# Performance work log

Hardware: AMD Instinct MI355X
Metric: run time of the kernel (lower is better)

The kernel has to match this reference:

```python
import jax, jax.numpy as jnp
import numpy as np

N_NODES = 100_000
N_EDGES = 3_200_000
FAN_IN, FAN_MID, FAN_OUT = 512, 256, 64
NEG_SLOPE = 0.01  # F.leaky_relu default


def setup_inputs() -> dict:
    key = jax.random.key(0)
    ks = jax.random.split(key, 8)
    x = jax.random.normal(ks[0], (N_NODES, FAN_IN), dtype=jnp.float32)
    edge_src = jax.random.randint(ks[1], (N_EDGES,), 0, N_NODES, dtype=jnp.int32)
    edge_dst = jax.random.randint(ks[2], (N_EDGES,), 0, N_NODES, dtype=jnp.int32)
    edge_w1 = jax.random.uniform(ks[3], (N_EDGES,), dtype=jnp.float32)
    edge_w2 = jax.random.uniform(ks[4], (N_EDGES,), dtype=jnp.float32)
    W1 = jax.random.normal(ks[5], (FAN_IN, FAN_MID), dtype=jnp.float32) * (1.0 / np.sqrt(FAN_IN))
    b1 = jnp.zeros((FAN_MID,), dtype=jnp.float32)
    W2 = jax.random.normal(ks[6], (FAN_MID, FAN_OUT), dtype=jnp.float32) * (1.0 / np.sqrt(FAN_MID))
    b2 = jnp.zeros((FAN_OUT,), dtype=jnp.float32)
    return {"x": x, "edge_src": edge_src, "edge_dst": edge_dst,
            "edge_w1": edge_w1, "edge_w2": edge_w2,
            "W1": W1, "b1": b1, "W2": W2, "b2": b2}


def _gcn_layer(x, W, b, src, dst, ew):
    # GraphConvolution: support = x @ W ; out = A @ support + b (A sparse via edges)
    support = x @ W                                 # [N, F_out]
    msgs = support[src] * ew[:, None]               # gather + scale, [E, F_out]
    agg = jax.ops.segment_sum(msgs, dst, num_segments=x.shape[0])  # scatter-add
    return agg + b


def reference(x, edge_src, edge_dst, edge_w1, edge_w2, W1, b1, W2, b2):
    h = _gcn_layer(x, W1, b1, edge_src, edge_dst, edge_w1)
    h = jax.nn.leaky_relu(h, NEG_SLOPE)
    # dropout is identity at inference (training=False)
    h = _gcn_layer(h, W2, b2, edge_src, edge_dst, edge_w2)
    return jax.nn.log_softmax(h, axis=1)
```

## Files before the change

kernel.cpp:

```cpp
#include <hip/hip_runtime.h>
#include <stdint.h>

#define FAN_IN  512
#define FAN_MID 256
#define FAN_OUT 64
#define NEG_SLOPE 0.01f
#define NPB 128
#define MAXNB 1024
#define BPART 256

typedef __bf16 bf16_t;
typedef bf16_t bf16x8 __attribute__((ext_vector_type(8)));
typedef float  f32x4  __attribute__((ext_vector_type(4)));
typedef unsigned short u16x8 __attribute__((ext_vector_type(8)));

__device__ inline unsigned short f2b(float f) {
    union { float f; unsigned int u; } v; v.f = f;
    unsigned int u = v.u;
    return (unsigned short)((u + 0x7fffu + ((u >> 16) & 1u)) >> 16);
}
__device__ inline float b2f(unsigned short u) {
    union { unsigned int u; float f; } v; v.u = ((unsigned int)u) << 16; return v.f;
}

__global__ void zerob_kernel(int* p, int n) {
    int i = blockIdx.x * 256 + threadIdx.x;
    if (i < n) p[i] = 0;
}

__global__ __launch_bounds__(256) void part_hist(const int* __restrict__ dst,
                                                 int* __restrict__ gcount,
                                                 int* __restrict__ bcount,
                                                 int E, int nb, int chunk) {
    __shared__ int lc[MAXNB];
    int blk = blockIdx.x;
    for (int i = threadIdx.x; i < nb; i += 256) lc[i] = 0;
    __syncthreads();
    int s = blk * chunk;
    int e = s + chunk; if (e > E) e = E;
    for (int i = s + threadIdx.x; i < e; i += 256)
        atomicAdd(&lc[dst[i] >> 7], 1);
    __syncthreads();
    for (int i = threadIdx.x; i < nb; i += 256) {
        int c = lc[i];
        gcount[blk * nb + i] = c;
        if (c) atomicAdd(&bcount[i], c);
    }
}

__global__ void bscan_kernel(const int* __restrict__ bcount, int* __restrict__ boff,
                             int nb, int E) {
    __shared__ int part[1024];
    int t = threadIdx.x;
    int chunk = (nb + 1023) >> 10;
    int s = t * chunk;
    int e = s + chunk; if (e > nb) e = nb;
    int sum = 0;
    for (int i = s; i < e; i++) sum += bcount[i];
    part[t] = sum;
    __syncthreads();
    for (int off = 1; off < 1024; off <<= 1) {
        int v = (t >= off) ? part[t - off] : 0;
        __syncthreads();
        part[t] += v;
        __syncthreads();
    }
    int run = (t == 0) ? 0 : part[t - 1];
    for (int i = s; i < e; i++) {
        boff[i] = run;
        run += bcount[i];
    }
    if (t == 1023) boff[nb] = E;
}

__global__ __launch_bounds__(BPART) void part_scan(const int* __restrict__ gcount,
                                                   const int* __restrict__ boff,
                                                   int* __restrict__ gbase, int nb) {
    __shared__ int v[BPART];
    int bucket = blockIdx.x;
    int t = threadIdx.x;
    int val = gcount[t * nb + bucket];
    v[t] = val;
    __syncthreads();
    for (int off = 1; off < BPART; off <<= 1) {
        int x = (t >= off) ? v[t - off] : 0;
        __syncthreads();
        v[t] += x;
        __syncthreads();
    }
    gbase[t * nb + bucket] = (t == 0 ? 0 : v[t - 1]) + boff[bucket];
}

__global__ __launch_bounds__(256) void part_scatter(const int* __restrict__ src,
                                                    const int* __restrict__ dst,
                                                    const float* __restrict__ w1,
                                                    const float* __restrict__ w2,
                                                    const int* __restrict__ gbase,
                                                    uint4* __restrict__ bstage,
                                                    int E, int nb, int chunk) {
    __shared__ int lcur[MAXNB];
    int blk = blockIdx.x;
    for (int i = threadIdx.x; i < nb; i += 256) lcur[i] = gbase[blk * nb + i];
    __syncthreads();
    int s = blk * chunk;
    int e = s + chunk; if (e > E) e = E;
    for (int i = s + threadIdx.x; i < e; i += 256) {
        int d = dst[i];
        int pos = atomicAdd(&lcur[d >> 7], 1);
        uint4 v;
        v.x = (unsigned int)src[i];
        v.y = __float_as_uint(w1[i]);
        v.z = __float_as_uint(w2[i]);
        v.w = (unsigned int)d;
        bstage[pos] = v;
    }
}

__global__ __launch_bounds__(256) void bsort_kernel(const uint4* __restrict__ bstage,
                                                    const int* __restrict__ boff,
                                                    int* __restrict__ offsets,
                                                    uint2* __restrict__ csr1,
                                                    uint2* __restrict__ csr2,
                                                    int Nn, int E, int nb) {
    __shared__ int cnt[NPB];
    __shared__ int scn[NPB];
    __shared__ int cur[NPB];
    int b = blockIdx.x;
    int t = threadIdx.x;
    int base = boff[b], end = boff[b + 1];
    int n0 = b * NPB;
    if (t < NPB) cnt[t] = 0;
    __syncthreads();
    for (int i = base + t; i < end; i += 256)
        atomicAdd(&cnt[bstage[i].w - n0], 1);
    __syncthreads();
    if (t == 0) {
        int run = 0;
        for (int j = 0; j < NPB; j++) { scn[j] = run; run += cnt[j]; }
    }
    __syncthreads();
    if (t < NPB) {
        cur[t] = scn[t];
        int n = n0 + t;
        if (n < Nn) offsets[n] = base + scn[t];
    }
    if (b == nb - 1 && t == 0) offsets[Nn] = E;
    __syncthreads();
    for (int i = base + t; i < end; i += 256) {
        uint4 rec = bstage[i];
        int lp = atomicAdd(&cur[rec.w - n0], 1);
        uint2 r1; r1.x = rec.x; r1.y = rec.y;
        uint2 r2; r2.x = rec.x; r2.y = rec.z;
        csr1[base + lp] = r1;
        csr2[base + lp] = r2;
    }
}

__global__ void convert_w_kernel(const float* __restrict__ W, unsigned short* __restrict__ Wt,
                                 int K, int N) {
    int idx = blockIdx.x * 256 + threadIdx.x;
    if (idx >= K * N) return;
    int k = idx / N, n = idx % N;
    Wt[(size_t)n * K + k] = f2b(W[idx]);
}

template<int K, int N, bool A_F32>
__global__ __launch_bounds__(256) void gemm_bt(const void* __restrict__ Ap,
                                               const unsigned short* __restrict__ Bt,
                                               unsigned short* __restrict__ C, int M) {
    constexpr int LDT = 40;
    constexpr int NW  = N / 64;
    __shared__ unsigned short As[64 * LDT];
    __shared__ unsigned short Bs[N * LDT];
    const int m0   = blockIdx.x * 64;
    const int tid  = threadIdx.x;
    const int lane = tid & 63;
    const int w    = tid >> 6;
    const int lrow = tid >> 2;
    const int lseg = (tid & 3) * 8;
    const int q    = lane >> 4;
    const int mm   = lane & 15;

    f32x4 acc[4][NW] = {};

    for (int k0 = 0; k0 < K; k0 += 32) {
        __syncthreads();
        {
            int gm = m0 + lrow;
            u16x8 av;
            if (A_F32) {
                const float* A32 = (const float*)Ap;
                if (gm < M) {
                    const float4* pp = (const float4*)(A32 + (size_t)gm * K + k0 + lseg);
                    float4 f0 = pp[0], f1 = pp[1];
                    av[0] = f2b(f0.x); av[1] = f2b(f0.y); av[2] = f2b(f0.z); av[3] = f2b(f0.w);
                    av[4] = f2b(f1.x); av[5] = f2b(f1.y); av[6] = f2b(f1.z); av[7] = f2b(f1.w);
                } else av = (u16x8)0;
            } else {
                const unsigned short* A16 = (const unsigned short*)Ap;
                if (gm < M) av = *(const u16x8*)(A16 + (size_t)gm * K + k0 + lseg);
                else        av = (u16x8)0;
            }
            *(u16x8*)&As[lrow * LDT + lseg] = av;
        }
#pragma unroll
        for (int r = 0; r < N / 64; r++) {
            int nr = r * 64 + lrow;
            *(u16x8*)&Bs[nr * LDT + lseg] =
                *(const u16x8*)(Bt + (size_t)nr * K + k0 + lseg);
        }
        __syncthreads();

        bf16x8 a[4], b[NW];
#pragma unroll
        for (int mi = 0; mi < 4; mi++)
            a[mi] = *(const bf16x8*)&As[(mi * 16 + mm) * LDT + q * 8];
#pragma unroll
        for (int ni = 0; ni < NW; ni++)
            b[ni] = *(const bf16x8*)&Bs[(w * NW * 16 + ni * 16 + mm) * LDT + q * 8];
#pragma unroll
        for (int mi = 0; mi < 4; mi++)
#pragma unroll
            for (int ni = 0; ni < NW; ni++)
                acc[mi][ni] = __builtin_amdgcn_mfma_f32_16x16x32_bf16(a[mi], b[ni], acc[mi][ni], 0, 0, 0);
    }

#pragma unroll
    for (int mi = 0; mi < 4; mi++)
#pragma unroll
        for (int ni = 0; ni < NW; ni++)
#pragma unroll
            for (int r = 0; r < 4; r++) {
                int row = m0 + mi * 16 + q * 4 + r;
                if (row < M)
                    C[(size_t)row * N + w * NW * 16 + ni * 16 + mm] = f2b(acc[mi][ni][r]);
            }
}

__global__ __launch_bounds__(256) void agg1_kernel(const unsigned short* __restrict__ S,
                                                   const int* __restrict__ offsets,
                                                   const uint2* __restrict__ edges,
                                                   const float* __restrict__ b1,
                                                   unsigned short* __restrict__ h, int Nn) {
    int wave = threadIdx.x >> 6;
    int lane = threadIdx.x & 63;
    int node = blockIdx.x * 4 + wave;
    if (node >= Nn) return;
    int s = offsets[node], e = offsets[node + 1];
    const int half = lane >> 5;
    const int elo  = lane & 31;
    float acc[8] = {0.f, 0.f, 0.f, 0.f, 0.f, 0.f, 0.f, 0.f};
    int i = s;
    for (; i + 16 <= e; i += 16) {
        uint2 ed[8];
#pragma unroll
        for (int p = 0; p < 8; p++) ed[p] = edges[i + 2 * p + half];
        u16x8 v[8];
#pragma unroll
        for (int p = 0; p < 8; p++)
            v[p] = *(const u16x8*)(S + (size_t)ed[p].x * 256 + elo * 8);
#pragma unroll
        for (int p = 0; p < 8; p++) {
            float w = __uint_as_float(ed[p].y);
#pragma unroll
            for (int k = 0; k < 8; k++) acc[k] += w * b2f(v[p][k]);
        }
    }
    for (; i + 2 <= e; i += 2) {
        uint2 ev = edges[i + half];
        float w = __uint_as_float(ev.y);
        u16x8 v = *(const u16x8*)(S + (size_t)ev.x * 256 + elo * 8);
#pragma unroll
        for (int k = 0; k < 8; k++) acc[k] += w * b2f(v[k]);
    }
    if (i < e) {
        uint2 ev = edges[i];
        float w = half ? 0.f : __uint_as_float(ev.y);
        u16x8 v = *(const u16x8*)(S + (size_t)ev.x * 256 + elo * 8);
#pragma unroll
        for (int k = 0; k < 8; k++) acc[k] += w * b2f(v[k]);
    }
#pragma unroll
    for (int k = 0; k < 8; k++) acc[k] += __shfl_xor(acc[k], 32);
    if (half == 0) {
        float4 bb0 = ((const float4*)b1)[elo * 2];
        float4 bb1 = ((const float4*)b1)[elo * 2 + 1];
        float r[8];
        r[0] = acc[0] + bb0.x; r[1] = acc[1] + bb0.y;
        r[2] = acc[2] + bb0.z; r[3] = acc[3] + bb0.w;
        r[4] = acc[4] + bb1.x; r[5] = acc[5] + bb1.y;
        r[6] = acc[6] + bb1.z; r[7] = acc[7] + bb1.w;
        u16x8 o;
#pragma unroll
        for (int k = 0; k < 8; k++) {
            float t = r[k] > 0.f ? r[k] : r[k] * NEG_SLOPE;
            o[k] = f2b(t);
        }
        *(u16x8*)&h[(size_t)node * 256 + elo * 8] = o;
    }
}

__global__ __launch_bounds__(256) void agg2_kernel(const unsigned short* __restrict__ S,
                                                   const int* __restrict__ offsets,
                                                   const uint2* __restrict__ edges,
                                                   const float* __restrict__ b2,
                                                   float* __restrict__ out, int Nn) {
    int wave = threadIdx.x >> 6;
    int lane = threadIdx.x & 63;
    int node = blockIdx.x * 4 + wave;
    if (node >= Nn) return;
    int s = offsets[node], e = offsets[node + 1];
    const int slot = lane >> 3;
    const int fblk = lane & 7;
    float acc[8] = {0.f, 0.f, 0.f, 0.f, 0.f, 0.f, 0.f, 0.f};
    int i = s;
    for (; i + 16 <= e; i += 16) {
        uint2 e0 = edges[i + slot];
        uint2 e1 = edges[i + 8 + slot];
        u16x8 v0 = *(const u16x8*)(S + (size_t)e0.x * 64 + fblk * 8);
        u16x8 v1 = *(const u16x8*)(S + (size_t)e1.x * 64 + fblk * 8);
        float w0 = __uint_as_float(e0.y), w1 = __uint_as_float(e1.y);
#pragma unroll
        for (int k = 0; k < 8; k++) acc[k] += w0 * b2f(v0[k]) + w1 * b2f(v1[k]);
    }
    for (; i + 8 <= e; i += 8) {
        uint2 ev = edges[i + slot];
        u16x8 v = *(const u16x8*)(S + (size_t)ev.x * 64 + fblk * 8);
        float w = __uint_as_float(ev.y);
#pragma unroll
        for (int k = 0; k < 8; k++) acc[k] += w * b2f(v[k]);
    }
    int rem = e - i;
    if (rem > 0) {
        int j = i + (slot < rem ? slot : rem - 1);
        uint2 ev = edges[j];
        float w = (slot < rem) ? __uint_as_float(ev.y) : 0.f;
        u16x8 v = *(const u16x8*)(S + (size_t)ev.x * 64 + fblk * 8);
#pragma unroll
        for (int k = 0; k < 8; k++) acc[k] += w * b2f(v[k]);
    }
#pragma unroll
    for (int k = 0; k < 8; k++) {
        acc[k] += __shfl_xor(acc[k], 8);
        acc[k] += __shfl_xor(acc[k], 16);
        acc[k] += __shfl_xor(acc[k], 32);
    }
    float4 bb0 = ((const float4*)b2)[fblk * 2];
    float4 bb1 = ((const float4*)b2)[fblk * 2 + 1];
    float logit[8];
    logit[0] = acc[0] + bb0.x; logit[1] = acc[1] + bb0.y;
    logit[2] = acc[2] + bb0.z; logit[3] = acc[3] + bb0.w;
    logit[4] = acc[4] + bb1.x; logit[5] = acc[5] + bb1.y;
    logit[6] = acc[6] + bb1.z; logit[7] = acc[7] + bb1.w;
    float m = logit[0];
#pragma unroll
    for (int k = 1; k < 8; k++) m = fmaxf(m, logit[k]);
    m = fmaxf(m, __shfl_xor(m, 1));
    m = fmaxf(m, __shfl_xor(m, 2));
    m = fmaxf(m, __shfl_xor(m, 4));
    float sum = 0.f;
#pragma unroll
    for (int k = 0; k < 8; k++) sum += expf(logit[k] - m);
    sum += __shfl_xor(sum, 1);
    sum += __shfl_xor(sum, 2);
    sum += __shfl_xor(sum, 4);
    float ls = logf(sum);
    if (slot == 0) {
        float* op = out + (size_t)node * 64 + fblk * 8;
        float4 o0, o1;
        o0.x = logit[0] - m - ls; o0.y = logit[1] - m - ls;
        o0.z = logit[2] - m - ls; o0.w = logit[3] - m - ls;
        o1.x = logit[4] - m - ls; o1.y = logit[5] - m - ls;
        o1.z = logit[6] - m - ls; o1.w = logit[7] - m - ls;
        ((float4*)op)[0] = o0;
        ((float4*)op)[1] = o1;
    }
}

extern "C" void kernel_launch(void* const* d_in, const int* in_sizes, int n_in,
                              void* d_out, int out_size, void* d_ws, size_t ws_size,
                              hipStream_t stream) {
    const float* x    = (const float*)d_in[0];
    const int*   esrc = (const int*)d_in[1];
    const int*   edst = (const int*)d_in[2];
    const float* ew1  = (const float*)d_in[3];
    const float* ew2  = (const float*)d_in[4];
    const float* W1   = (const float*)d_in[5];
    const float* b1   = (const float*)d_in[6];
    const float* W2   = (const float*)d_in[7];
    const float* b2   = (const float*)d_in[8];
    float* out = (float*)d_out;
    const int Nn = in_sizes[0] / FAN_IN;
    const int E  = in_sizes[1];
    const int NB = (Nn + NPB - 1) / NPB;
    const int chunk = (E + BPART - 1) / BPART;

    char* p = (char*)d_ws;
    auto alloc = [&](size_t bytes) -> char* {
        char* r = p;
        p += (bytes + 255) & ~(size_t)255;
        return r;
    };
    size_t s1_bytes = (size_t)Nn * FAN_MID * 2;
    size_t st_bytes = (size_t)E * 16;
    char* s1_region = alloc(s1_bytes > st_bytes ? s1_bytes : st_bytes);
    unsigned short* support1 = (unsigned short*)s1_region;
    uint4*          bstage   = (uint4*)s1_region;
    unsigned short* h        = (unsigned short*)alloc((size_t)Nn * FAN_MID * 2);
    unsigned short* support2 = (unsigned short*)alloc((size_t)Nn * FAN_OUT * 2);
    unsigned short* W1t      = (unsigned short*)alloc((size_t)FAN_IN * FAN_MID * 2);
    unsigned short* W2t      = (unsigned short*)alloc((size_t)FAN_MID * FAN_OUT * 2);
    int*            bcount   = (int*)alloc((size_t)NB * 4);
    int*            boff     = (int*)alloc(((size_t)NB + 1) * 4);
    int*            gcount   = (int*)alloc((size_t)BPART * NB * 4);
    int*            gbase    = (int*)alloc((size_t)BPART * NB * 4);
    int*            offsets  = (int*)alloc(((size_t)Nn + 1) * 4);
    uint2*          csr1     = (uint2*)alloc((size_t)E * 8);
    uint2*          csr2     = (uint2*)alloc((size_t)E * 8);

    zerob_kernel<<<(NB + 255) / 256, 256, 0, stream>>>(bcount, NB);
    part_hist<<<BPART, 256, 0, stream>>>(edst, gcount, bcount, E, NB, chunk);
    bscan_kernel<<<1, 1024, 0, stream>>>(bcount, boff, NB, E);
    part_scan<<<NB, BPART, 0, stream>>>(gcount, boff, gbase, NB);
    part_scatter<<<BPART, 256, 0, stream>>>(esrc, edst, ew1, ew2, gbase, bstage, E, NB, chunk);
    bsort_kernel<<<NB, 256, 0, stream>>>(bstage, boff, offsets, csr1, csr2, Nn, E, NB);

    convert_w_kernel<<<(FAN_IN * FAN_MID + 255) / 256, 256, 0, stream>>>(W1, W1t, FAN_IN, FAN_MID);
    convert_w_kernel<<<(FAN_MID * FAN_OUT + 255) / 256, 256, 0, stream>>>(W2, W2t, FAN_MID, FAN_OUT);

    gemm_bt<FAN_IN, FAN_MID, true><<<dim3((Nn + 63) / 64, 1), 256, 0, stream>>>(
        x, W1t, support1, Nn);
    agg1_kernel<<<(Nn + 3) / 4, 256, 0, stream>>>(support1, offsets, csr1, b1, h, Nn);

    gemm_bt<FAN_MID, FAN_OUT, false><<<dim3((Nn + 63) / 64, 1), 256, 0, stream>>>(
        h, W2t, support2, Nn);
    agg2_kernel<<<(Nn + 3) / 4, 256, 0, stream>>>(support2, offsets, csr2, b2, out, Nn);
}
```

Before: 829.6 us.

## Fuse second-layer GEMM into first aggregation and simplify CSR build

The two-level bucketed partition sort is replaced by a direct per-node counting sort. It uses a global atomic histogram, a single-block scan, and an atomic scatter straight into the two CSR arrays. The first aggregation kernel now has each wave process 4 nodes, stage the activated hidden rows in LDS, and multiply them by W2 with MFMA. This removes the separate h buffer and the second GEMM launch, and with them the write and re-read of the hidden activations through global memory. In exchange, each MFMA tile uses only 4 of its 16 rows, each wave walks 4 nodes serially, and global atomics may contend more in the sort.

New measurement: 1.220 ms. 47.1% more time.

```diff
diff --git a/kernel.cpp b/kernel.cpp
--- a/kernel.cpp
+++ b/kernel.cpp
@@ -5,9 +5,6 @@
 #define FAN_MID 256
 #define FAN_OUT 64
 #define NEG_SLOPE 0.01f
-#define NPB 128
-#define MAXNB 1024
-#define BPART 256
 
 typedef __bf16 bf16_t;
 typedef bf16_t bf16x8 __attribute__((ext_vector_type(8)));
@@ -23,40 +20,26 @@
     union { unsigned int u; float f; } v; v.u = ((unsigned int)u) << 16; return v.f;
 }
 
-__global__ void zerob_kernel(int* p, int n) {
+__global__ void zero_kernel(int* p, int n) {
     int i = blockIdx.x * 256 + threadIdx.x;
     if (i < n) p[i] = 0;
 }
 
-__global__ __launch_bounds__(256) void part_hist(const int* __restrict__ dst,
-                                                 int* __restrict__ gcount,
-                                                 int* __restrict__ bcount,
-                                                 int E, int nb, int chunk) {
-    __shared__ int lc[MAXNB];
-    int blk = blockIdx.x;
-    for (int i = threadIdx.x; i < nb; i += 256) lc[i] = 0;
-    __syncthreads();
-    int s = blk * chunk;
-    int e = s + chunk; if (e > E) e = E;
-    for (int i = s + threadIdx.x; i < e; i += 256)
-        atomicAdd(&lc[dst[i] >> 7], 1);
-    __syncthreads();
-    for (int i = threadIdx.x; i < nb; i += 256) {
-        int c = lc[i];
-        gcount[blk * nb + i] = c;
-        if (c) atomicAdd(&bcount[i], c);
-    }
-}
-
-__global__ void bscan_kernel(const int* __restrict__ bcount, int* __restrict__ boff,
-                             int nb, int E) {
+__global__ __launch_bounds__(256) void hist_n(const int* __restrict__ dst,
+                                              int* __restrict__ cnt, int E) {
+    int i = blockIdx.x * 256 + threadIdx.x;
+    if (i < E) atomicAdd(&cnt[dst[i]], 1);
+}
+
+__global__ void scan_n(const int* __restrict__ cnt, int* __restrict__ offsets,
+                       int* __restrict__ cur, int Nn, int E) {
     __shared__ int part[1024];
     int t = threadIdx.x;
-    int chunk = (nb + 1023) >> 10;
+    int chunk = (Nn + 1023) >> 10;
     int s = t * chunk;
-    int e = s + chunk; if (e > nb) e = nb;
+    int e = s + chunk; if (e > Nn) e = Nn;
     int sum = 0;
-    for (int i = s; i < e; i++) sum += bcount[i];
+    for (int i = s; i < e; i++) sum += cnt[i];
     part[t] = sum;
     __syncthreads();
     for (int off = 1; off < 1024; off <<= 1) {
@@ -67,93 +50,28 @@
     }
     int run = (t == 0) ? 0 : part[t - 1];
     for (int i = s; i < e; i++) {
-        boff[i] = run;
-        run += bcount[i];
-    }
-    if (t == 1023) boff[nb] = E;
-}
-
-__global__ __launch_bounds__(BPART) void part_scan(const int* __restrict__ gcount,
-                                                   const int* __restrict__ boff,
-                                                   int* __restrict__ gbase, int nb) {
-    __shared__ int v[BPART];
-    int bucket = blockIdx.x;
-    int t = threadIdx.x;
-    int val = gcount[t * nb + bucket];
-    v[t] = val;
-    __syncthreads();
-    for (int off = 1; off < BPART; off <<= 1) {
-        int x = (t >= off) ? v[t - off] : 0;
-        __syncthreads();
-        v[t] += x;
-        __syncthreads();
-    }
-    gbase[t * nb + bucket] = (t == 0 ? 0 : v[t - 1]) + boff[bucket];
-}
-
-__global__ __launch_bounds__(256) void part_scatter(const int* __restrict__ src,
-                                                    const int* __restrict__ dst,
-                                                    const float* __restrict__ w1,
-                                                    const float* __restrict__ w2,
-                                                    const int* __restrict__ gbase,
-                                                    uint4* __restrict__ bstage,
-                                                    int E, int nb, int chunk) {
-    __shared__ int lcur[MAXNB];
-    int blk = blockIdx.x;
-    for (int i = threadIdx.x; i < nb; i += 256) lcur[i] = gbase[blk * nb + i];
-    __syncthreads();
-    int s = blk * chunk;
-    int e = s + chunk; if (e > E) e = E;
-    for (int i = s + threadIdx.x; i < e; i += 256) {
-        int d = dst[i];
-        int pos = atomicAdd(&lcur[d >> 7], 1);
-        uint4 v;
-        v.x = (unsigned int)src[i];
-        v.y = __float_as_uint(w1[i]);
-        v.z = __float_as_uint(w2[i]);
-        v.w = (unsigned int)d;
-        bstage[pos] = v;
-    }
-}
-
-__global__ __launch_bounds__(256) void bsort_kernel(const uint4* __restrict__ bstage,
-                                                    const int* __restrict__ boff,
-                                                    int* __restrict__ offsets,
-                                                    uint2* __restrict__ csr1,
-                                                    uint2* __restrict__ csr2,
-                                                    int Nn, int E, int nb) {
-    __shared__ int cnt[NPB];
-    __shared__ int scn[NPB];
-    __shared__ int cur[NPB];
-    int b = blockIdx.x;
-    int t = threadIdx.x;
-    int base = boff[b], end = boff[b + 1];
-    int n0 = b * NPB;
-    if (t < NPB) cnt[t] = 0;
-    __syncthreads();
-    for (int i = base + t; i < end; i += 256)
-        atomicAdd(&cnt[bstage[i].w - n0], 1);
-    __syncthreads();
-    if (t == 0) {
-        int run = 0;
-        for (int j = 0; j < NPB; j++) { scn[j] = run; run += cnt[j]; }
-    }
-    __syncthreads();
-    if (t < NPB) {
-        cur[t] = scn[t];
-        int n = n0 + t;
-        if (n < Nn) offsets[n] = base + scn[t];
-    }
-    if (b == nb - 1 && t == 0) offsets[Nn] = E;
-    __syncthreads();
-    for (int i = base + t; i < end; i += 256) {
-        uint4 rec = bstage[i];
-        int lp = atomicAdd(&cur[rec.w - n0], 1);
-        uint2 r1; r1.x = rec.x; r1.y = rec.y;
-        uint2 r2; r2.x = rec.x; r2.y = rec.z;
-        csr1[base + lp] = r1;
-        csr2[base + lp] = r2;
-    }
+        offsets[i] = run;
+        cur[i] = run;
+        run += cnt[i];
+    }
+    if (t == 1023) offsets[Nn] = E;
+}
+
+__global__ __launch_bounds__(256) void scatter_n(const int* __restrict__ src,
+                                                 const int* __restrict__ dst,
+                                                 const float* __restrict__ w1,
+                                                 const float* __restrict__ w2,
+                                                 int* __restrict__ cur,
+                                                 uint2* __restrict__ csr1,
+                                                 uint2* __restrict__ csr2, int E) {
+    int i = blockIdx.x * 256 + threadIdx.x;
+    if (i >= E) return;
+    int d = dst[i];
+    int pos = atomicAdd(&cur[d], 1);
+    uint2 r1; r1.x = (unsigned int)src[i]; r1.y = __float_as_uint(w1[i]);
+    uint2 r2; r2.x = (unsigned int)src[i]; r2.y = __float_as_uint(w2[i]);
+    csr1[pos] = r1;
+    csr2[pos] = r2;
 }
 
 __global__ void convert_w_kernel(const float* __restrict__ W, unsigned short* __restrict__ Wt,
@@ -237,66 +155,97 @@
             }
 }
 
-__global__ __launch_bounds__(256) void agg1_kernel(const unsigned short* __restrict__ S,
-                                                   const int* __restrict__ offsets,
-                                                   const uint2* __restrict__ edges,
-                                                   const float* __restrict__ b1,
-                                                   unsigned short* __restrict__ h, int Nn) {
-    int wave = threadIdx.x >> 6;
+__global__ __launch_bounds__(256) void agg1_fused(const unsigned short* __restrict__ S,
+                                                  const int* __restrict__ offsets,
+                                                  const uint2* __restrict__ edges,
+                                                  const float* __restrict__ b1,
+                                                  const unsigned short* __restrict__ W2t,
+                                                  unsigned short* __restrict__ S2, int Nn) {
+    __shared__ unsigned short Hs[4][16][264];
+    int wv   = threadIdx.x >> 6;
     int lane = threadIdx.x & 63;
-    int node = blockIdx.x * 4 + wave;
-    if (node >= Nn) return;
-    int s = offsets[node], e = offsets[node + 1];
     const int half = lane >> 5;
     const int elo  = lane & 31;
-    float acc[8] = {0.f, 0.f, 0.f, 0.f, 0.f, 0.f, 0.f, 0.f};
-    int i = s;
-    for (; i + 16 <= e; i += 16) {
-        uint2 ed[8];
-#pragma unroll
-        for (int p = 0; p < 8; p++) ed[p] = edges[i + 2 * p + half];
-        u16x8 v[8];
-#pragma unroll
-        for (int p = 0; p < 8; p++)
-            v[p] = *(const u16x8*)(S + (size_t)ed[p].x * 256 + elo * 8);
-#pragma unroll
-        for (int p = 0; p < 8; p++) {
-            float w = __uint_as_float(ed[p].y);
-#pragma unroll
-            for (int k = 0; k < 8; k++) acc[k] += w * b2f(v[p][k]);
-        }
-    }
-    for (; i + 2 <= e; i += 2) {
-        uint2 ev = edges[i + half];
-        float w = __uint_as_float(ev.y);
-        u16x8 v = *(const u16x8*)(S + (size_t)ev.x * 256 + elo * 8);
-#pragma unroll
-        for (int k = 0; k < 8; k++) acc[k] += w * b2f(v[k]);
-    }
-    if (i < e) {
-        uint2 ev = edges[i];
-        float w = half ? 0.f : __uint_as_float(ev.y);
-        u16x8 v = *(const u16x8*)(S + (size_t)ev.x * 256 + elo * 8);
-#pragma unroll
-        for (int k = 0; k < 8; k++) acc[k] += w * b2f(v[k]);
-    }
-#pragma unroll
-    for (int k = 0; k < 8; k++) acc[k] += __shfl_xor(acc[k], 32);
-    if (half == 0) {
-        float4 bb0 = ((const float4*)b1)[elo * 2];
-        float4 bb1 = ((const float4*)b1)[elo * 2 + 1];
-        float r[8];
-        r[0] = acc[0] + bb0.x; r[1] = acc[1] + bb0.y;
-        r[2] = acc[2] + bb0.z; r[3] = acc[3] + bb0.w;
-        r[4] = acc[4] + bb1.x; r[5] = acc[5] + bb1.y;
-        r[6] = acc[6] + bb1.z; r[7] = acc[7] + bb1.w;
-        u16x8 o;
-#pragma unroll
-        for (int k = 0; k < 8; k++) {
-            float t = r[k] > 0.f ? r[k] : r[k] * NEG_SLOPE;
-            o[k] = f2b(t);
-        }
-        *(u16x8*)&h[(size_t)node * 256 + elo * 8] = o;
+    const int q    = lane >> 4;
+    const int mm   = lane & 15;
+    int nodeBase = blockIdx.x * 16 + wv * 4;
+
+    for (int nl = 0; nl < 4; nl++) {
+        int node = nodeBase + nl;
+        if (node >= Nn) break;
+        int s = offsets[node], e = offsets[node + 1];
+        float acc[8] = {0.f, 0.f, 0.f, 0.f, 0.f, 0.f, 0.f, 0.f};
+        int i = s;
+        for (; i + 16 <= e; i += 16) {
+            uint2 ed[8];
+#pragma unroll
+            for (int p = 0; p < 8; p++) ed[p] = edges[i + 2 * p + half];
+            u16x8 v[8];
+#pragma unroll
+            for (int p = 0; p < 8; p++)
+                v[p] = *(const u16x8*)(S + (size_t)ed[p].x * 256 + elo * 8);
+#pragma unroll
+            for (int p = 0; p < 8; p++) {
+                float w = __uint_as_float(ed[p].y);
+#pragma unroll
+                for (int k = 0; k < 8; k++) acc[k] += w * b2f(v[p][k]);
+            }
+        }
+        for (; i + 2 <= e; i += 2) {
+            uint2 ev = edges[i + half];
+            float w = __uint_as_float(ev.y);
+            u16x8 v = *(const u16x8*)(S + (size_t)ev.x * 256 + elo * 8);
+#pragma unroll
+            for (int k = 0; k < 8; k++) acc[k] += w * b2f(v[k]);
+        }
+        if (i < e) {
+            uint2 ev = edges[i];
+            float w = half ? 0.f : __uint_as_float(ev.y);
+            u16x8 v = *(const u16x8*)(S + (size_t)ev.x * 256 + elo * 8);
+#pragma unroll
+            for (int k = 0; k < 8; k++) acc[k] += w * b2f(v[k]);
+        }
+#pragma unroll
+        for (int k = 0; k < 8; k++) acc[k] += __shfl_xor(acc[k], 32);
+        if (half == 0) {
+            float4 bb0 = ((const float4*)b1)[elo * 2];
+            float4 bb1 = ((const float4*)b1)[elo * 2 + 1];
+            float r[8];
+            r[0] = acc[0] + bb0.x; r[1] = acc[1] + bb0.y;
+            r[2] = acc[2] + bb0.z; r[3] = acc[3] + bb0.w;
+            r[4] = acc[4] + bb1.x; r[5] = acc[5] + bb1.y;
+            r[6] = acc[6] + bb1.z; r[7] = acc[7] + bb1.w;
+            u16x8 o;
+#pragma unroll
+            for (int k = 0; k < 8; k++) {
+                float t = r[k] > 0.f ? r[k] : r[k] * NEG_SLOPE;
+                o[k] = f2b(t);
+            }
+            *(u16x8*)&Hs[wv][nl][elo * 8] = o;
+        }
+    }
+    asm volatile("s_waitcnt lgkmcnt(0)" ::: "memory");
+
+    f32x4 acc2[4] = {};
+#pragma unroll
+    for (int ks = 0; ks < 8; ks++) {
+        bf16x8 a = *(const bf16x8*)&Hs[wv][mm][ks * 32 + q * 8];
+#pragma unroll
+        for (int ni = 0; ni < 4; ni++) {
+            bf16x8 b = *(const bf16x8*)(W2t + (size_t)(ni * 16 + mm) * 256 + ks * 32 + q * 8);
+            acc2[ni] = __builtin_amdgcn_mfma_f32_16x16x32_bf16(a, b, acc2[ni], 0, 0, 0);
+        }
+    }
+    if (q == 0) {
+#pragma unroll
+        for (int r = 0; r < 4; r++) {
+            int node = nodeBase + r;
+            if (node < Nn) {
+#pragma unroll
+                for (int ni = 0; ni < 4; ni++)
+                    S2[(size_t)node * 64 + ni * 16 + mm] = f2b(acc2[ni][r]);
+            }
+        }
     }
 }
 
@@ -392,8 +341,6 @@
     float* out = (float*)d_out;
     const int Nn = in_sizes[0] / FAN_IN;
     const int E  = in_sizes[1];
-    const int NB = (Nn + NPB - 1) / NPB;
-    const int chunk = (E + BPART - 1) / BPART;
 
     char* p = (char*)d_ws;
     auto alloc = [&](size_t bytes) -> char* {
@@ -401,38 +348,30 @@
         p += (bytes + 255) & ~(size_t)255;
         return r;
     };
-    size_t s1_bytes = (size_t)Nn * FAN_MID * 2;
-    size_t st_bytes = (size_t)E * 16;
-    char* s1_region = alloc(s1_bytes > st_bytes ? s1_bytes : st_bytes);
-    unsigned short* support1 = (unsigned short*)s1_region;
-    uint4*          bstage   = (uint4*)s1_region;
-    unsigned short* h        = (unsigned short*)alloc((size_t)Nn * FAN_MID * 2);
+    unsigned short* support1 = (unsigned short*)alloc((size_t)Nn * FAN_MID * 2);
     unsigned short* support2 = (unsigned short*)alloc((size_t)Nn * FAN_OUT * 2);
     unsigned short* W1t      = (unsigned short*)alloc((size_t)FAN_IN * FAN_MID * 2);
     unsigned short* W2t      = (unsigned short*)alloc((size_t)FAN_MID * FAN_OUT * 2);
-    int*            bcount   = (int*)alloc((size_t)NB * 4);
-    int*            boff     = (int*)alloc(((size_t)NB + 1) * 4);
-    int*            gcount   = (int*)alloc((size_t)BPART * NB * 4);
-    int*            gbase    = (int*)alloc((size_t)BPART * NB * 4);
+    int*            cnt      = (int*)alloc((size_t)Nn * 4);
+    int*            cur      = (int*)alloc((size_t)Nn * 4);
     int*            offsets  = (int*)alloc(((size_t)Nn + 1) * 4);
     uint2*          csr1     = (uint2*)alloc((size_t)E * 8);
     uint2*          csr2     = (uint2*)alloc((size_t)E * 8);
 
-    zerob_kernel<<<(NB + 255) / 256, 256, 0, stream>>>(bcount, NB);
-    part_hist<<<BPART, 256, 0, stream>>>(edst, gcount, bcount, E, NB, chunk);
-    bscan_kernel<<<1, 1024, 0, stream>>>(bcount, boff, NB, E);
-    part_scan<<<NB, BPART, 0, stream>>>(gcount, boff, gbase, NB);
-    part_scatter<<<BPART, 256, 0, stream>>>(esrc, edst, ew1, ew2, gbase, bstage, E, NB, chunk);
-    bsort_kernel<<<NB, 256, 0, stream>>>(bstage, boff, offsets, csr1, csr2, Nn, E, NB);
+    const int EB = (E + 255) / 256;
+
+    zero_kernel<<<(Nn + 255) / 256, 256, 0, stream>>>(cnt, Nn);
+    hist_n<<<EB, 256, 0, stream>>>(edst, cnt, E);
+    scan_n<<<1, 1024, 0, stream>>>(cnt, offsets, cur, Nn, E);
+    scatter_n<<<EB, 256, 0, stream>>>(esrc, edst, ew1, ew2, cur, csr1, csr2, E);
 
     convert_w_kernel<<<(FAN_IN * FAN_MID + 255) / 256, 256, 0, stream>>>(W1, W1t, FAN_IN, FAN_MID);
     convert_w_kernel<<<(FAN_MID * FAN_OUT + 255) / 256, 256, 0, stream>>>(W2, W2t, FAN_MID, FAN_OUT);
 
     gemm_bt<FAN_IN, FAN_MID, true><<<dim3((Nn + 63) / 64, 1), 256, 0, stream>>>(
         x, W1t, support1, Nn);
-    agg1_kernel<<<(Nn + 3) / 4, 256, 0, stream>>>(support1, offsets, csr1, b1, h, Nn);
-
-    gemm_bt<FAN_MID, FAN_OUT, false><<<dim3((Nn + 63) / 64, 1), 256, 0, stream>>>(
-        h, W2t, support2, Nn);
+
+    agg1_fused<<<(Nn + 15) / 16, 256, 0, stream>>>(support1, offsets, csr1, b1, W2t, support2, Nn);
+
     agg2_kernel<<<(Nn + 3) / 4, 256, 0, stream>>>(support2, offsets, csr2, b2, out, Nn);
 }
```

## Fuse layer-1 aggregation with layer-2 GEMM via shared-memory tile and MFMA

Applied to the files above, without the earlier changes.

The first-layer aggregation kernel now processes 16 nodes per block (4 per wave, sequentially), stages the leaky-ReLU bf16 hidden rows in shared memory, then multiplies them by W2 with MFMA to write support2 directly. This removes the intermediate h buffer round-trip and the separate second GEMM launch. In exchange each wave handles four nodes serially, which may reduce memory-level parallelism in the gather phase, and W2t is reloaded from global/L2 per block.

Measured after the change: 825.3 us. No clear change (-0.5%).

```diff
diff --git a/kernel.cpp b/kernel.cpp
--- a/kernel.cpp
+++ b/kernel.cpp
@@ -237,66 +237,89 @@
             }
 }
 
-__global__ __launch_bounds__(256) void agg1_kernel(const unsigned short* __restrict__ S,
-                                                   const int* __restrict__ offsets,
-                                                   const uint2* __restrict__ edges,
-                                                   const float* __restrict__ b1,
-                                                   unsigned short* __restrict__ h, int Nn) {
-    int wave = threadIdx.x >> 6;
+__global__ __launch_bounds__(256) void agg1_fused(const unsigned short* __restrict__ S,
+                                                  const int* __restrict__ offsets,
+                                                  const uint2* __restrict__ edges,
+                                                  const float* __restrict__ b1,
+                                                  const unsigned short* __restrict__ W2t,
+                                                  unsigned short* __restrict__ S2, int Nn) {
+    __shared__ unsigned short Hs[16][264];
+    int wv   = threadIdx.x >> 6;
     int lane = threadIdx.x & 63;
-    int node = blockIdx.x * 4 + wave;
-    if (node >= Nn) return;
-    int s = offsets[node], e = offsets[node + 1];
     const int half = lane >> 5;
     const int elo  = lane & 31;
-    float acc[8] = {0.f, 0.f, 0.f, 0.f, 0.f, 0.f, 0.f, 0.f};
-    int i = s;
-    for (; i + 16 <= e; i += 16) {
-        uint2 ed[8];
-#pragma unroll
-        for (int p = 0; p < 8; p++) ed[p] = edges[i + 2 * p + half];
-        u16x8 v[8];
-#pragma unroll
-        for (int p = 0; p < 8; p++)
-            v[p] = *(const u16x8*)(S + (size_t)ed[p].x * 256 + elo * 8);
-#pragma unroll
-        for (int p = 0; p < 8; p++) {
-            float w = __uint_as_float(ed[p].y);
-#pragma unroll
-            for (int k = 0; k < 8; k++) acc[k] += w * b2f(v[p][k]);
-        }
-    }
-    for (; i + 2 <= e; i += 2) {
-        uint2 ev = edges[i + half];
-        float w = __uint_as_float(ev.y);
-        u16x8 v = *(const u16x8*)(S + (size_t)ev.x * 256 + elo * 8);
-#pragma unroll
-        for (int k = 0; k < 8; k++) acc[k] += w * b2f(v[k]);
-    }
-    if (i < e) {
-        uint2 ev = edges[i];
-        float w = half ? 0.f : __uint_as_float(ev.y);
-        u16x8 v = *(const u16x8*)(S + (size_t)ev.x * 256 + elo * 8);
-#pragma unroll
-        for (int k = 0; k < 8; k++) acc[k] += w * b2f(v[k]);
-    }
-#pragma unroll
-    for (int k = 0; k < 8; k++) acc[k] += __shfl_xor(acc[k], 32);
-    if (half == 0) {
-        float4 bb0 = ((const float4*)b1)[elo * 2];
-        float4 bb1 = ((const float4*)b1)[elo * 2 + 1];
-        float r[8];
-        r[0] = acc[0] + bb0.x; r[1] = acc[1] + bb0.y;
-        r[2] = acc[2] + bb0.z; r[3] = acc[3] + bb0.w;
-        r[4] = acc[4] + bb1.x; r[5] = acc[5] + bb1.y;
-        r[6] = acc[6] + bb1.z; r[7] = acc[7] + bb1.w;
-        u16x8 o;
-#pragma unroll
-        for (int k = 0; k < 8; k++) {
-            float t = r[k] > 0.f ? r[k] : r[k] * NEG_SLOPE;
-            o[k] = f2b(t);
-        }
-        *(u16x8*)&h[(size_t)node * 256 + elo * 8] = o;
+    const int q    = lane >> 4;
+    const int mm   = lane & 15;
+    const int node0 = blockIdx.x * 16;
+
+    for (int nl = 0; nl < 4; nl++) {
+        int node = node0 + wv * 4 + nl;
+        int s = 0, e = 0;
+        if (node < Nn) { s = offsets[node]; e = offsets[node + 1]; }
+        float acc[8] = {0.f, 0.f, 0.f, 0.f, 0.f, 0.f, 0.f, 0.f};
+        int i = s;
+        for (; i + 16 <= e; i += 16) {
+            uint2 ed[8];
+#pragma unroll
+            for (int p = 0; p < 8; p++) ed[p] = edges[i + 2 * p + half];
+            u16x8 v[8];
+#pragma unroll
+            for (int p = 0; p < 8; p++)
+                v[p] = *(const u16x8*)(S + (size_t)ed[p].x * 256 + elo * 8);
+#pragma unroll
+            for (int p = 0; p < 8; p++) {
+                float w = __uint_as_float(ed[p].y);
+#pragma unroll
+                for (int k = 0; k < 8; k++) acc[k] += w * b2f(v[p][k]);
+            }
+        }
+        for (; i + 2 <= e; i += 2) {
+            uint2 ev = edges[i + half];
+            float w = __uint_as_float(ev.y);
+            u16x8 v = *(const u16x8*)(S + (size_t)ev.x * 256 + elo * 8);
+#pragma unroll
+            for (int k = 0; k < 8; k++) acc[k] += w * b2f(v[k]);
+        }
+        if (i < e) {
+            uint2 ev = edges[i];
+            float w = half ? 0.f : __uint_as_float(ev.y);
+            u16x8 v = *(const u16x8*)(S + (size_t)ev.x * 256 + elo * 8);
+#pragma unroll
+            for (int k = 0; k < 8; k++) acc[k] += w * b2f(v[k]);
+        }
+#pragma unroll
+        for (int k = 0; k < 8; k++) acc[k] += __shfl_xor(acc[k], 32);
+        if (half == 0) {
+            float4 bb0 = ((const float4*)b1)[elo * 2];
+            float4 bb1 = ((const float4*)b1)[elo * 2 + 1];
+            float r[8];
+            r[0] = acc[0] + bb0.x; r[1] = acc[1] + bb0.y;
+            r[2] = acc[2] + bb0.z; r[3] = acc[3] + bb0.w;
+            r[4] = acc[4] + bb1.x; r[5] = acc[5] + bb1.y;
+            r[6] = acc[6] + bb1.z; r[7] = acc[7] + bb1.w;
+            u16x8 o;
+#pragma unroll
+            for (int k = 0; k < 8; k++) {
+                float t = r[k] > 0.f ? r[k] : r[k] * NEG_SLOPE;
+                o[k] = f2b(t);
+            }
+            *(u16x8*)&Hs[wv * 4 + nl][elo * 8] = o;
+        }
+    }
+    __syncthreads();
+
+    f32x4 acc2 = {};
+#pragma unroll
+    for (int ks = 0; ks < 8; ks++) {
+        bf16x8 a = *(const bf16x8*)&Hs[mm][ks * 32 + q * 8];
+        bf16x8 b = *(const bf16x8*)(W2t + (size_t)(wv * 16 + mm) * 256 + ks * 32 + q * 8);
+        acc2 = __builtin_amdgcn_mfma_f32_16x16x32_bf16(a, b, acc2, 0, 0, 0);
+    }
+#pragma unroll
+    for (int r = 0; r < 4; r++) {
+        int node = node0 + q * 4 + r;
+        if (node < Nn)
+            S2[(size_t)node * 64 + wv * 16 + mm] = f2b(acc2[r]);
     }
 }
 
@@ -406,7 +429,6 @@
     char* s1_region = alloc(s1_bytes > st_bytes ? s1_bytes : st_bytes);
     unsigned short* support1 = (unsigned short*)s1_region;
     uint4*          bstage   = (uint4*)s1_region;
-    unsigned short* h        = (unsigned short*)alloc((size_t)Nn * FAN_MID * 2);
     unsigned short* support2 = (unsigned short*)alloc((size_t)Nn * FAN_OUT * 2);
     unsigned short* W1t      = (unsigned short*)alloc((size_t)FAN_IN * FAN_MID * 2);
     unsigned short* W2t      = (unsigned short*)alloc((size_t)FAN_MID * FAN_OUT * 2);
@@ -430,9 +452,8 @@
 
     gemm_bt<FAN_IN, FAN_MID, true><<<dim3((Nn + 63) / 64, 1), 256, 0, stream>>>(
         x, W1t, support1, Nn);
-    agg1_kernel<<<(Nn + 3) / 4, 256, 0, stream>>>(support1, offsets, csr1, b1, h, Nn);
-
-    gemm_bt<FAN_MID, FAN_OUT, false><<<dim3((Nn + 63) / 64, 1), 256, 0, stream>>>(
-        h, W2t, support2, Nn);
+
+    agg1_fused<<<(Nn + 15) / 16, 256, 0, stream>>>(support1, offsets, csr1, b1, W2t, support2, Nn);
+
     agg2_kernel<<<(Nn + 3) / 4, 256, 0, stream>>>(support2, offsets, csr2, b2, out, Nn);
 }
```
